# Kernel optimization log

Hardware: AMD Instinct MI355X
Metric: run time of the kernel (lower is better)

## Reference

```python
import jax, jax.numpy as jnp
import numpy as np

B, FR, D = 32, 300, 2048
E, G, K = 2, 8, 64
FEAT = E * D // G          # 512
VLAD = K * FEAT            # 32768
H, R = 2048, 8
NC = 3862
BN_EPS = 1e-5
L2_EPS = 1e-12


def _bn(x, g, b, m, v):
    # eval-mode BatchNorm1d with running stats
    return (x - m) * jax.lax.rsqrt(v + BN_EPS) * g + b


def _l2n(x, axis):
    # torch F.normalize: x / max(||x||, eps)
    n = jnp.sqrt(jnp.sum(x * x, axis=axis, keepdims=True))
    return x / jnp.maximum(n, L2_EPS)


def setup_inputs() -> dict:
    key = jax.random.key(0)
    ks = jax.random.split(key, 10)
    rn = lambda k, s: jax.random.normal(k, s, jnp.float32) * 0.02
    return {
        "x": jax.random.normal(ks[0], (B, FR, D), jnp.float32),
        "fc1_w": rn(ks[1], (E * D, D)), "fc1_b": jnp.zeros((E * D,), jnp.float32),
        "fc2_w": rn(ks[2], (G, E * D)), "fc2_b": jnp.zeros((G,), jnp.float32),
        "c1": jax.random.uniform(ks[3], (E * D, G * K), jnp.float32),
        "c2": jax.random.uniform(ks[4], (1, FEAT, K), jnp.float32),
        "bn1_g": jnp.ones((G * K,), jnp.float32), "bn1_b": jnp.zeros((G * K,), jnp.float32),
        "bn1_m": jnp.zeros((G * K,), jnp.float32), "bn1_v": jnp.ones((G * K,), jnp.float32),
        "bn2_g": jnp.ones((VLAD,), jnp.float32), "bn2_b": jnp.zeros((VLAD,), jnp.float32),
        "bn2_m": jnp.zeros((VLAD,), jnp.float32), "bn2_v": jnp.ones((VLAD,), jnp.float32),
        "cgf_w": rn(ks[5], (H, VLAD)), "cgf_b": jnp.zeros((H,), jnp.float32),
        "cgbn_g": jnp.ones((H,), jnp.float32), "cgbn_b": jnp.zeros((H,), jnp.float32),
        "cgbn_m": jnp.zeros((H,), jnp.float32), "cgbn_v": jnp.ones((H,), jnp.float32),
        "g1_w": rn(ks[6], (H // R, H)), "g1_b": jnp.zeros((H // R,), jnp.float32),
        "gbn_g": jnp.ones((H // R,), jnp.float32), "gbn_b": jnp.zeros((H // R,), jnp.float32),
        "gbn_m": jnp.zeros((H // R,), jnp.float32), "gbn_v": jnp.ones((H // R,), jnp.float32),
        "g2_w": rn(ks[7], (H, H // R)), "g2_b": jnp.zeros((H,), jnp.float32),
        "fc3_w": rn(ks[8], (NC, H)), "fc3_b": jnp.zeros((NC,), jnp.float32),
    }


def _forward(x, fc1_w, fc1_b, fc2_w, fc2_b, c1, c2,
             bn1_g, bn1_b, bn1_m, bn1_v, bn2_g, bn2_b, bn2_m, bn2_v,
             cgf_w, cgf_b, cgbn_g, cgbn_b, cgbn_m, cgbn_v,
             g1_w, g1_b, gbn_g, gbn_b, gbn_m, gbn_v, g2_w, g2_b, fc3_w, fc3_b):
    b, fr, d = x.shape
    xn = _l2n(x, 2)                                      # per-frame L2 normalize
    h = xn @ fc1_w.T + fc1_b                             # [B,FR,E*D]
    att = jax.nn.sigmoid(h @ fc2_w.T + fc2_b)            # [B,FR,G]
    att = att.reshape(b, fr * G, 1)
    act = jnp.einsum('bfd,dc->bfc', h, c1)               # [B,FR,G*K]
    act = _bn(act, bn1_g, bn1_b, bn1_m, bn1_v)
    act = act.reshape(b, fr * G, K)
    act = jax.nn.softmax(act, axis=-1) * att             # soft-assign * attention
    a = act.sum(axis=1, keepdims=True) * c2              # [B,FEAT,K] via broadcast
    res = h.reshape(b, fr * G, FEAT)
    vlad = jnp.einsum('bnk,bnf->bfk', act, res) - a      # [B,FEAT,K]
    vlad = _l2n(vlad, 1).reshape(b, VLAD)                # intra-norm, flatten feat-major
    vlad = _bn(vlad, bn2_g, bn2_b, bn2_m, bn2_v)
    # SE context gating (dropout identity in reference)
    y = _bn(vlad @ cgf_w.T + cgf_b, cgbn_g, cgbn_b, cgbn_m, cgbn_v)   # [B,H]
    gate = jax.nn.sigmoid(
        jax.nn.relu(_bn(y @ g1_w.T + g1_b, gbn_g, gbn_b, gbn_m, gbn_v)) @ g2_w.T + g2_b)
    return (y * gate) @ fc3_w.T + fc3_b                  # [B,NC]


def reference(x, fc1_w, fc1_b, fc2_w, fc2_b, c1, c2,
              bn1_g, bn1_b, bn1_m, bn1_v, bn2_g, bn2_b, bn2_m, bn2_v,
              cgf_w, cgf_b, cgbn_g, cgbn_b, cgbn_m, cgbn_v,
              g1_w, g1_b, gbn_g, gbn_b, gbn_m, gbn_v, g2_w, g2_b, fc3_w, fc3_b):
    return _forward(x, fc1_w, fc1_b, fc2_w, fc2_b, c1, c2,
                    bn1_g, bn1_b, bn1_m, bn1_v, bn2_g, bn2_b, bn2_m, bn2_v,
                    cgf_w, cgf_b, cgbn_g, cgbn_b, cgbn_m, cgbn_v,
                    g1_w, g1_b, gbn_g, gbn_b, gbn_m, gbn_v, g2_w, g2_b, fc3_w, fc3_b)
```

## Files before the change

### kernel.cpp

```cpp
#include <hip/hip_runtime.h>

typedef unsigned short u16;
typedef unsigned int u32;
using f32x4 = __attribute__((ext_vector_type(4))) float;
using s16x8 = __attribute__((ext_vector_type(8))) short;
using u16x4 = __attribute__((ext_vector_type(4))) u16;

#define DEV __device__ __forceinline__

DEV float bf2f(u16 u) { union { u32 i; float f; } v; v.i = ((u32)u) << 16; return v.f; }
DEV u16 f2bf(float f) {
  union { float ff; u32 uu; } v; v.ff = f;
  u32 r = (v.uu + 0x7fffu + ((v.uu >> 16) & 1u)) >> 16;
  return (u16)r;
}

DEV void gl_lds16(const void* g, void* l) {
  __builtin_amdgcn_global_load_lds(
      (const __attribute__((address_space(1))) u32*)g,
      (__attribute__((address_space(3))) u32*)l, 16, 0, 0);
}

__global__ __launch_bounds__(256) void k_l2norm(const float* __restrict__ x, u16* __restrict__ xn) {
  int r = blockIdx.x, t = threadIdx.x;
  const float* xr = x + (size_t)r * 2048;
  float v[8], s = 0.f;
#pragma unroll
  for (int i = 0; i < 8; i++) { v[i] = xr[t + i*256]; s += v[i]*v[i]; }
#pragma unroll
  for (int off = 32; off > 0; off >>= 1) s += __shfl_xor(s, off, 64);
  __shared__ float red[4];
  if ((t & 63) == 0) red[t >> 6] = s;
  __syncthreads();
  float inv = 1.f / fmaxf(sqrtf(red[0]+red[1]+red[2]+red[3]), 1e-12f);
  u16* xo = xn + (size_t)r * 2048;
#pragma unroll
  for (int i = 0; i < 8; i++) xo[t + i*256] = f2bf(v[i]*inv);
}

__global__ void k_cvt(const float* __restrict__ in, u16* __restrict__ out, int n4) {
  int i = blockIdx.x*256 + threadIdx.x, st = gridDim.x*256;
  for (; i < n4; i += st) {
    f32x4 v = ((const f32x4*)in)[i];
    u16x4 o;
    o[0] = f2bf(v[0]); o[1] = f2bf(v[1]); o[2] = f2bf(v[2]); o[3] = f2bf(v[3]);
    ((u16x4*)out)[i] = o;
  }
}

__global__ __launch_bounds__(256) void k_transpose(const float* __restrict__ c1, u16* __restrict__ c1t) {
  __shared__ float tile[32][33];
  int k0 = blockIdx.x*32, n0 = blockIdx.y*32;
  int tx = threadIdx.x & 31, ty = threadIdx.x >> 5;
  for (int i = ty; i < 32; i += 8) tile[i][tx] = c1[(size_t)(k0+i)*512 + n0 + tx];
  __syncthreads();
  for (int i = ty; i < 32; i += 8) c1t[(size_t)(n0+i)*4096 + k0 + tx] = f2bf(tile[tx][i]);
}

template<bool WF32, bool WBF16>
__global__ __launch_bounds__(256) void k_gemm(
    const u16* __restrict__ A, const u16* __restrict__ Bt, const float* __restrict__ bias,
    float* __restrict__ Cf, u16* __restrict__ Cb, int N, int K, int Nlim,
    int MT, int NT, int swz) {
  __shared__ u16 As[128*32];
  __shared__ u16 Bs[128*32];
  int bid = blockIdx.x, mt, nt;
  if (swz) {
    int mg = (MT + 7) >> 3;
    int gid = bid >> 5, gl = bid & 31;
    mt = (gid % mg)*8 + (gl & 7);
    nt = (gid / mg)*4 + (gl >> 3);
    if (mt >= MT) return;
  } else { mt = bid % MT; nt = bid / MT; }
  int t = threadIdx.x, wv = t >> 6;
  int quad = (t & 63) >> 4, lr = t & 15;
  size_t m0 = (size_t)mt * 128, n0 = (size_t)nt * 128;
  int wm = wv & 1, wn = wv >> 1;
  int srow = t >> 2;
  int scol = (((t & 3) ^ ((t >> 3) & 3)) * 8);
  const u16* gA = A + (m0 + srow)*(size_t)K + scol;
  const u16* gB = Bt + (n0 + srow)*(size_t)K + scol;
  u16* lA = &As[wv*512];
  u16* lB = &Bs[wv*512];
  int xq = (quad ^ ((lr >> 1) & 3)) * 8;
  f32x4 acc[4][4];
#pragma unroll
  for (int i = 0; i < 4; i++)
#pragma unroll
    for (int j = 0; j < 4; j++) acc[i][j] = (f32x4){0.f,0.f,0.f,0.f};
  for (int k0 = 0; k0 < K; k0 += 32) {
    gl_lds16(gA + k0, lA);
    gl_lds16(gA + (size_t)64*K + k0, lA + 2048);
    gl_lds16(gB + k0, lB);
    gl_lds16(gB + (size_t)64*K + k0, lB + 2048);
    __syncthreads();
    s16x8 af[4], bfr[4];
#pragma unroll
    for (int i = 0; i < 4; i++) {
      af[i]  = *(const s16x8*)&As[(wm*64 + i*16 + lr)*32 + xq];
      bfr[i] = *(const s16x8*)&Bs[(wn*64 + i*16 + lr)*32 + xq];
    }
#pragma unroll
    for (int i = 0; i < 4; i++)
#pragma unroll
      for (int j = 0; j < 4; j++)
        acc[i][j] = __builtin_amdgcn_mfma_f32_16x16x32_bf16(af[i], bfr[j], acc[i][j], 0, 0, 0);
    __syncthreads();
  }
#pragma unroll
  for (int j = 0; j < 4; j++) {
    size_t nn = n0 + wn*64 + j*16 + lr;
    if ((int)nn >= Nlim) continue;
    float bj = bias ? bias[nn] : 0.f;
#pragma unroll
    for (int i = 0; i < 4; i++) {
      size_t mr = m0 + wm*64 + i*16 + quad*4;
#pragma unroll
      for (int r = 0; r < 4; r++) {
        float v = acc[i][j][r] + bj;
        if (WF32)  Cf[(mr + r)*N + nn] = v;
        if (WBF16) Cb[(mr + r)*N + nn] = f2bf(v);
      }
    }
  }
}

__global__ __launch_bounds__(256) void k_hbt(const u16* __restrict__ hb, u16* __restrict__ hbT) {
  __shared__ u16 tile[64*33];
  int nt = blockIdx.x, ft = blockIdx.y, b = blockIdx.z, t = threadIdx.x;
  int n0 = nt*32, f0 = ft*64;
  int rrel = t >> 6, g = (t >> 3) & 7, fi = (t & 7)*8;
  const u16* src = hb + ((size_t)(b*300 + (n0 >> 3) + rrel))*4096 + g*512 + f0 + fi;
  u16 v[8];
  *(u16x4*)v = *(const u16x4*)src;
  *(u16x4*)(v+4) = *(const u16x4*)(src+4);
  int nl = rrel*8 + g;
#pragma unroll
  for (int e = 0; e < 8; e++) tile[(fi+e)*33 + nl] = v[e];
  __syncthreads();
  int f = t >> 2, nc = (t & 3)*8;
  u16 o[8];
#pragma unroll
  for (int e = 0; e < 8; e++) o[e] = tile[f*33 + nc + e];
  u16* dst = hbT + ((size_t)b*512 + f0 + f)*2400 + n0 + nc;
  *(u16x4*)dst = *(u16x4*)o;
  *(u16x4*)(dst+4) = *(u16x4*)(o+4);
}

__global__ __launch_bounds__(512) void k_softmax(const float* __restrict__ act_ext,
    const float* __restrict__ fc2_b,
    const float* __restrict__ g, const float* __restrict__ b,
    const float* __restrict__ mu, const float* __restrict__ var, u16* __restrict__ actT) {
  int m = blockIdx.x, t = threadIdx.x;
  int bb = m / 300, fr = m - bb*300;
  int gi = t >> 6, k = t & 63, c = t;
  float v = act_ext[(size_t)m*640 + c];
  v = (v - mu[c]) * rsqrtf(var[c] + 1e-5f) * g[c] + b[c];
  float mx = v;
#pragma unroll
  for (int off = 32; off > 0; off >>= 1) mx = fmaxf(mx, __shfl_xor(mx, off, 64));
  float e = __expf(v - mx);
  float s = e;
#pragma unroll
  for (int off = 32; off > 0; off >>= 1) s += __shfl_xor(s, off, 64);
  float attl = act_ext[(size_t)m*640 + 512 + gi] + fc2_b[gi];
  float attv = 1.f / (1.f + __expf(-attl));
  float r = (e / s) * attv;
  __shared__ u16 st[64*9];
  st[k*9 + gi] = f2bf(r);
  __syncthreads();
  if (t < 64) {
    u16 o[8];
#pragma unroll
    for (int e2 = 0; e2 < 8; e2++) o[e2] = st[t*9 + e2];
    u16* dst = actT + ((size_t)bb*64 + t)*2400 + fr*8;
    *(u16x4*)dst = *(u16x4*)o;
    *(u16x4*)(dst+4) = *(u16x4*)(o+4);
  }
}

__global__ __launch_bounds__(256) void k_asum(const u16* __restrict__ actT, float* __restrict__ a_sum) {
  int b = blockIdx.x, t = threadIdx.x;
  int k = t >> 2, q = t & 3;
  const u16* p = actT + ((size_t)b*64 + k)*2400 + q*600;
  float acc = 0.f;
  for (int j = 0; j < 600; j += 8) {
    u16x4 a0 = *(const u16x4*)(p + j);
    u16x4 a1 = *(const u16x4*)(p + j + 4);
    acc += bf2f(a0[0])+bf2f(a0[1])+bf2f(a0[2])+bf2f(a0[3])
         + bf2f(a1[0])+bf2f(a1[1])+bf2f(a1[2])+bf2f(a1[3]);
  }
  __shared__ float red[256];
  red[t] = acc;
  __syncthreads();
  if (t < 64) a_sum[b*64 + t] = red[t*4] + red[t*4+1] + red[t*4+2] + red[t*4+3];
}

__global__ __launch_bounds__(256) void k_vlad(const u16* __restrict__ hbT, const u16* __restrict__ actT,
                                              float* __restrict__ P2) {
  __shared__ u16 As[128*32];
  __shared__ u16 Bs[64*32];
  int t = threadIdx.x, wv = t >> 6;
  int quad = (t & 63) >> 4, lr = t & 15;
  int ft = blockIdx.x, b = blockIdx.y, ns = blockIdx.z;
  int wm = wv & 1, wn = wv >> 1;
  int srow = t >> 2;
  int scol = (((t & 3) ^ ((t >> 3) & 3)) * 8);
  int xq = (quad ^ ((lr >> 1) & 3)) * 8;
  const u16* gA = hbT + ((size_t)b*512 + ft*128 + srow)*2400 + ns*480 + scol;
  const u16* gB = actT + ((size_t)b*64 + srow)*2400 + ns*480 + scol;
  u16* lA = &As[wv*512];
  u16* lB = &Bs[wv*512];
  f32x4 acc[4][2];
#pragma unroll
  for (int i = 0; i < 4; i++)
#pragma unroll
    for (int j = 0; j < 2; j++) acc[i][j] = (f32x4){0.f,0.f,0.f,0.f};
  for (int k0 = 0; k0 < 480; k0 += 32) {
    gl_lds16(gA + k0, lA);
    gl_lds16(gA + (size_t)64*2400 + k0, lA + 2048);
    gl_lds16(gB + k0, lB);
    __syncthreads();
    s16x8 af[4], bfr[2];
#pragma unroll
    for (int i = 0; i < 4; i++)
      af[i] = *(const s16x8*)&As[(wm*64 + i*16 + lr)*32 + xq];
#pragma unroll
    for (int j = 0; j < 2; j++)
      bfr[j] = *(const s16x8*)&Bs[(wn*32 + j*16 + lr)*32 + xq];
#pragma unroll
    for (int i = 0; i < 4; i++)
#pragma unroll
      for (int j = 0; j < 2; j++)
        acc[i][j] = __builtin_amdgcn_mfma_f32_16x16x32_bf16(af[i], bfr[j], acc[i][j], 0, 0, 0);
    __syncthreads();
  }
  size_t base = ((size_t)ns*32 + b)*512*64;
#pragma unroll
  for (int j = 0; j < 2; j++) {
    int kc = wn*32 + j*16 + lr;
#pragma unroll
    for (int i = 0; i < 4; i++) {
      int f = ft*128 + wm*64 + i*16 + quad*4;
#pragma unroll
      for (int r = 0; r < 4; r++)
        P2[base + (size_t)(f + r)*64 + kc] = acc[i][j][r];
    }
  }
}

__global__ __launch_bounds__(256) void k_norm2(const float* __restrict__ P2, const float* __restrict__ a_sum,
    const float* __restrict__ c2, const float* __restrict__ g, const float* __restrict__ b,
    const float* __restrict__ mu, const float* __restrict__ var, float* __restrict__ out) {
  int k = blockIdx.x, bb = blockIdx.y, t = threadIdx.x;
  float as = a_sum[bb*64 + k];
  int f0 = t, f1 = t + 256;
  const size_t PS = (size_t)32*512*64;
  size_t base = (size_t)bb*512*64;
  float x0 = 0.f, x1 = 0.f;
#pragma unroll
  for (int ns = 0; ns < 5; ns++) {
    x0 += P2[ns*PS + base + (size_t)f0*64 + k];
    x1 += P2[ns*PS + base + (size_t)f1*64 + k];
  }
  x0 -= as * c2[f0*64 + k];
  x1 -= as * c2[f1*64 + k];
  float s = x0*x0 + x1*x1;
#pragma unroll
  for (int off = 32; off > 0; off >>= 1) s += __shfl_xor(s, off, 64);
  __shared__ float red[4];
  if ((t & 63) == 0) red[t >> 6] = s;
  __syncthreads();
  float inv = 1.f / fmaxf(sqrtf(red[0]+red[1]+red[2]+red[3]), 1e-12f);
  int c0 = f0*64 + k, c1 = f1*64 + k;
  out[(size_t)bb*32768 + c0] = (x0*inv - mu[c0]) * rsqrtf(var[c0]+1e-5f) * g[c0] + b[c0];
  out[(size_t)bb*32768 + c1] = (x1*inv - mu[c1]) * rsqrtf(var[c1]+1e-5f) * g[c1] + b[c1];
}

__global__ __launch_bounds__(256) void k_skgemm(
    const float* __restrict__ A, const float* __restrict__ W,
    float* __restrict__ P, int N, int K, int KC, int Npad) {
  constexpr int LDB = 72;
  __shared__ u16 Bs[128*LDB];
  __shared__ u16 As[32*LDB];
  int t = threadIdx.x;
  int wv = t >> 6, quad = (t & 63) >> 4, lr = t & 15;
  int n0 = blockIdx.x * 128;
  size_t kc0 = (size_t)blockIdx.y * KC;
  f32x4 acc[2][2];
#pragma unroll
  for (int i = 0; i < 2; i++)
#pragma unroll
    for (int j = 0; j < 2; j++) acc[i][j] = (f32x4){0.f,0.f,0.f,0.f};
  int wl[8]; size_t wg[8];
#pragma unroll
  for (int i = 0; i < 8; i++) {
    int slot = i*256 + t;
    int r = slot >> 4, q = slot & 15;
    int row = n0 + r; if (row >= N) row = N - 1;
    wl[i] = r*LDB + q*4;
    wg[i] = (size_t)row*K + kc0 + q*4;
  }
  int al[2]; size_t ag[2];
#pragma unroll
  for (int i = 0; i < 2; i++) {
    int slot = i*256 + t;
    int r = slot >> 4, q = slot & 15;
    al[i] = r*LDB + q*4;
    ag[i] = (size_t)r*K + kc0 + q*4;
  }
  int nst = KC >> 6;
  f32x4 wv4[8], av4[2];
#pragma unroll
  for (int i = 0; i < 8; i++) wv4[i] = *(const f32x4*)(W + wg[i]);
#pragma unroll
  for (int i = 0; i < 2; i++) av4[i] = *(const f32x4*)(A + ag[i]);
  for (int s = 0; s < nst; s++) {
    if (s) __syncthreads();
#pragma unroll
    for (int i = 0; i < 8; i++) {
      u16x4 o;
      o[0] = f2bf(wv4[i][0]); o[1] = f2bf(wv4[i][1]);
      o[2] = f2bf(wv4[i][2]); o[3] = f2bf(wv4[i][3]);
      *(u16x4*)&Bs[wl[i]] = o;
    }
#pragma unroll
    for (int i = 0; i < 2; i++) {
      u16x4 o;
      o[0] = f2bf(av4[i][0]); o[1] = f2bf(av4[i][1]);
      o[2] = f2bf(av4[i][2]); o[3] = f2bf(av4[i][3]);
      *(u16x4*)&As[al[i]] = o;
    }
    __syncthreads();
    if (s + 1 < nst) {
      int off = (s + 1) * 64;
#pragma unroll
      for (int i = 0; i < 8; i++) wv4[i] = *(const f32x4*)(W + wg[i] + off);
#pragma unroll
      for (int i = 0; i < 2; i++) av4[i] = *(const f32x4*)(A + ag[i] + off);
    }
#pragma unroll
    for (int ks = 0; ks < 2; ks++) {
      s16x8 af[2];
#pragma unroll
      for (int i = 0; i < 2; i++)
        af[i] = *(const s16x8*)&As[(i*16 + lr)*LDB + ks*32 + quad*8];
#pragma unroll
      for (int j = 0; j < 2; j++) {
        s16x8 bf = *(const s16x8*)&Bs[(wv*32 + j*16 + lr)*LDB + ks*32 + quad*8];
#pragma unroll
        for (int i = 0; i < 2; i++)
          acc[i][j] = __builtin_amdgcn_mfma_f32_16x16x32_bf16(af[i], bf, acc[i][j], 0, 0, 0);
      }
    }
  }
#pragma unroll
  for (int i = 0; i < 2; i++)
#pragma unroll
    for (int j = 0; j < 2; j++) {
      int n = n0 + wv*32 + j*16 + lr;
#pragma unroll
      for (int r = 0; r < 4; r++) {
        int m = i*16 + quad*4 + r;
        P[((size_t)blockIdx.y*32 + m)*Npad + n] = acc[i][j][r];
      }
    }
}

template<int EPI>
__global__ __launch_bounds__(256) void k_skred(const float* __restrict__ P, int KSPLIT, int N, int Npad,
    const float* __restrict__ bias, const float* __restrict__ bg, const float* __restrict__ bb,
    const float* __restrict__ bm, const float* __restrict__ bv, float* __restrict__ C) {
  int idx = blockIdx.x*256 + threadIdx.x;
  if (idx >= 32*N) return;
  int m = idx / N, n = idx - m*N;
  float s = 0.f;
  for (int k = 0; k < KSPLIT; k++) s += P[((size_t)k*32 + m)*Npad + n];
  float v = s + (bias ? bias[n] : 0.f);
  if (EPI == 1 || EPI == 2) {
    v = (v - bm[n]) * rsqrtf(bv[n] + 1e-5f) * bg[n] + bb[n];
    if (EPI == 2) v = fmaxf(v, 0.f);
  } else if (EPI == 3) {
    v = 1.f / (1.f + __expf(-v));
  }
  C[idx] = v;
}

__global__ void k_mul(const float* __restrict__ a, const float* __restrict__ b, float* __restrict__ o, int n) {
  int i = blockIdx.x*256 + threadIdx.x;
  if (i < n) o[i] = a[i]*b[i];
}

extern "C" void kernel_launch(void* const* d_in, const int* in_sizes, int n_in,
                              void* d_out, int out_size, void* d_ws, size_t ws_size,
                              hipStream_t stream) {
  (void)in_sizes; (void)n_in; (void)out_size; (void)ws_size;
  const float* x      = (const float*)d_in[0];
  const float* fc1_w  = (const float*)d_in[1];
  const float* fc1_b  = (const float*)d_in[2];
  const float* fc2_w  = (const float*)d_in[3];
  const float* fc2_b  = (const float*)d_in[4];
  const float* c1     = (const float*)d_in[5];
  const float* c2     = (const float*)d_in[6];
  const float* bn1_g  = (const float*)d_in[7];
  const float* bn1_b  = (const float*)d_in[8];
  const float* bn1_m  = (const float*)d_in[9];
  const float* bn1_v  = (const float*)d_in[10];
  const float* bn2_g  = (const float*)d_in[11];
  const float* bn2_b  = (const float*)d_in[12];
  const float* bn2_m  = (const float*)d_in[13];
  const float* bn2_v  = (const float*)d_in[14];
  const float* cgf_w  = (const float*)d_in[15];
  const float* cgf_b  = (const float*)d_in[16];
  const float* cgbn_g = (const float*)d_in[17];
  const float* cgbn_b = (const float*)d_in[18];
  const float* cgbn_m = (const float*)d_in[19];
  const float* cgbn_v = (const float*)d_in[20];
  const float* g1_w   = (const float*)d_in[21];
  const float* g1_b   = (const float*)d_in[22];
  const float* gbn_g  = (const float*)d_in[23];
  const float* gbn_b  = (const float*)d_in[24];
  const float* gbn_m  = (const float*)d_in[25];
  const float* gbn_v  = (const float*)d_in[26];
  const float* g2_w   = (const float*)d_in[27];
  const float* g2_b   = (const float*)d_in[28];
  const float* fc3_w  = (const float*)d_in[29];
  const float* fc3_b  = (const float*)d_in[30];

  char* w = (char*)d_ws;
  u16*   xn    = (u16*)  (w + 0);
  u16*   w1b   = (u16*)  (w + 39321600);
  u16*   hbT   = (u16*)  (w + 0);
  u16*   hb    = (u16*)  (w + 78643200);
  u16*   c1ext = (u16*)  (w + 157286400);
  float* actx  = (float*)(w + 162529280);
  u16*   actT  = (u16*)  (w + 187105280);
  float* P2    = (float*)(w + 196935680);
  float* P     = (float*)(w + 196935680);
  float* a_sum = (float*)(w + 217907200);
  float* vladn = (float*)(w + 217915392);
  float* y     = (float*)(w + 222109696);
  float* z     = (float*)(w + 222371840);
  float* gate  = (float*)(w + 222404608);
  float* yg    = (float*)(w + 222666752);

  k_l2norm<<<9600, 256, 0, stream>>>(x, xn);
  k_cvt<<<2048, 256, 0, stream>>>(fc1_w, w1b, (4096*2048)/4);
  k_transpose<<<dim3(128, 16), 256, 0, stream>>>(c1, c1ext);
  k_cvt<<<32, 256, 0, stream>>>(fc2_w, c1ext + (size_t)512*4096, (8*4096)/4);
  k_gemm<false, true><<<2560, 256, 0, stream>>>(xn, w1b, fc1_b, nullptr, hb, 4096, 2048, 4096, 75, 32, 1);
  k_hbt<<<dim3(75, 8, 32), 256, 0, stream>>>(hb, hbT);
  k_gemm<true, false><<<375, 256, 0, stream>>>(hb, c1ext, nullptr, actx, nullptr, 640, 4096, 520, 75, 5, 0);
  k_softmax<<<9600, 512, 0, stream>>>(actx, fc2_b, bn1_g, bn1_b, bn1_m, bn1_v, actT);
  k_asum<<<32, 256, 0, stream>>>(actT, a_sum);
  k_vlad<<<dim3(4, 32, 5), 256, 0, stream>>>(hbT, actT, P2);
  k_norm2<<<dim3(64, 32), 256, 0, stream>>>(P2, a_sum, c2, bn2_g, bn2_b, bn2_m, bn2_v, vladn);

  k_skgemm<<<dim3(16, 64), 256, 0, stream>>>(vladn, cgf_w, P, 2048, 32768, 512, 2048);
  k_skred<1><<<256, 256, 0, stream>>>(P, 64, 2048, 2048, cgf_b, cgbn_g, cgbn_b, cgbn_m, cgbn_v, y);
  k_skgemm<<<dim3(2, 32), 256, 0, stream>>>(y, g1_w, P, 256, 2048, 64, 256);
  k_skred<2><<<32, 256, 0, stream>>>(P, 32, 256, 256, g1_b, gbn_g, gbn_b, gbn_m, gbn_v, z);
  k_skgemm<<<dim3(16, 4), 256, 0, stream>>>(z, g2_w, P, 2048, 256, 64, 2048);
  k_skred<3><<<256, 256, 0, stream>>>(P, 4, 2048, 2048, g2_b, nullptr, nullptr, nullptr, nullptr, gate);
  k_mul<<<256, 256, 0, stream>>>(y, gate, yg, 65536);
  k_skgemm<<<dim3(31, 16), 256, 0, stream>>>(yg, fc3_w, P, 3862, 2048, 128, 3968);
  k_skred<0><<<483, 256, 0, stream>>>(P, 16, 3862, 3968, fc3_b, nullptr, nullptr, nullptr, nullptr, (float*)d_out);
}
```

Baseline: 1.012 ms.

## Add 256x256-tile 8-wave MFMA GEMM with ping-pong LDS for fc1

Adds a new bf16 MFMA GEMM kernel that uses 256x256 output tiles, 512 threads and double-buffered LDS filled by direct global-to-LDS loads. Loads are staggered across the K loop with explicit vmcnt waits, barriers and s_setprio around MFMA bursts. It replaces the 128-tile GEMM for the fc1 projection (9600x4096x2048). The aim is more data reuse per tile and better overlap of loads with MFMA work. In exchange it needs 128KB of LDS per block, which limits occupancy, and the last M tile reads A rows past the 9600 valid rows (stores are guarded).

```diff
diff --git a/kernel.cpp b/kernel.cpp
--- a/kernel.cpp
+++ b/kernel.cpp
@@ -20,6 +20,13 @@
       (const __attribute__((address_space(1))) u32*)g,
       (__attribute__((address_space(3))) u32*)l, 16, 0, 0);
 }
+
+DEV void BAR() { __builtin_amdgcn_s_barrier(); }
+DEV void LGKM0() { asm volatile("s_waitcnt lgkmcnt(0)" ::: "memory"); __builtin_amdgcn_sched_barrier(0); }
+DEV void VM6() { asm volatile("s_waitcnt vmcnt(6)" ::: "memory"); }
+DEV void VM0() { asm volatile("s_waitcnt vmcnt(0)" ::: "memory"); }
+DEV void PRIO1() { __builtin_amdgcn_s_setprio(1); }
+DEV void PRIO0() { __builtin_amdgcn_s_setprio(0); }
 
 __global__ __launch_bounds__(256) void k_l2norm(const float* __restrict__ x, u16* __restrict__ xn) {
   int r = blockIdx.x, t = threadIdx.x;
@@ -120,6 +127,131 @@
         float v = acc[i][j][r] + bj;
         if (WF32)  Cf[(mr + r)*N + nn] = v;
         if (WBF16) Cb[(mr + r)*N + nn] = f2bf(v);
+      }
+    }
+  }
+}
+
+template<bool WF32, bool WBF16>
+__global__ __launch_bounds__(512, 2) void k_gemm256(
+    const u16* __restrict__ A, const u16* __restrict__ Bt, const float* __restrict__ bias,
+    float* __restrict__ Cf, u16* __restrict__ Cb,
+    int M, int N, int K, int Nlim, int MT, int NT, int swz) {
+  constexpr int TILE = 256*64;
+  __shared__ u16 lds[4*TILE];
+  int bid = blockIdx.x;
+  if (swz) { int c = (MT*NT) >> 3; bid = (bid & 7)*c + (bid >> 3); }
+  int mt = bid % MT, nt = bid / MT;
+  int t = threadIdx.x, wv = t >> 6, lane = t & 63;
+  int quad = lane >> 4, lr = lane & 15;
+  int wm = wv >> 2, wn = wv & 3;
+  size_t m0 = (size_t)mt * 256, n0 = (size_t)nt * 256;
+  int srow = wv*8 + (lane >> 3);
+  int schunk = ((lane & 7) ^ (lane >> 3)) * 8;
+  const u16* gA = A  + (size_t)(m0 + srow)*K + schunk;
+  const u16* gB = Bt + (size_t)(n0 + srow)*K + schunk;
+  size_t row64 = (size_t)64 * K;
+  int lofs = wv*512;
+  int raBase = (wm*128 + lr)*64;
+  int rbBase = (wn*64  + lr)*64;
+  int pc0 = ((0 + quad) ^ (lr & 7)) * 8;
+  int pc1 = ((4 + quad) ^ (lr & 7)) * 8;
+  f32x4 acc[8][4];
+#pragma unroll
+  for (int i = 0; i < 8; i++)
+#pragma unroll
+    for (int j = 0; j < 4; j++) acc[i][j] = (f32x4){0.f,0.f,0.f,0.f};
+
+  int T = K >> 6;
+  u16* A0 = lds;            u16* B0 = lds + TILE;
+  u16* A1 = lds + 2*TILE;   u16* B1 = lds + 3*TILE;
+#pragma unroll
+  for (int q = 0; q < 4; q++) gl_lds16(gA + q*row64, A0 + q*4096 + lofs);
+#pragma unroll
+  for (int q = 0; q < 4; q++) gl_lds16(gB + q*row64, B0 + q*4096 + lofs);
+#pragma unroll
+  for (int q = 0; q < 4; q++) gl_lds16(gA + 64 + q*row64, A1 + q*4096 + lofs);
+  gl_lds16(gB + 64 + 0*row64, B1 + 0*4096 + lofs);
+  gl_lds16(gB + 64 + 1*row64, B1 + 1*4096 + lofs);
+  VM6();
+  BAR();
+
+  for (int tt = 0; tt < T; ++tt) {
+    u16* Ac = lds + (tt & 1)*(2*TILE);
+    u16* Bc = Ac + TILE;
+    u16* Bn = lds + ((tt + 1) & 1)*(2*TILE) + TILE;
+    s16x8 a[8], b[4];
+#pragma unroll
+    for (int i = 0; i < 8; i++) a[i] = *(const s16x8*)&Ac[raBase + i*1024 + pc0];
+#pragma unroll
+    for (int j = 0; j < 4; j++) b[j] = *(const s16x8*)&Bc[rbBase + j*1024 + pc0];
+    if (tt + 1 < T) {
+      const u16* gB1 = gB + (size_t)(tt + 1)*64;
+      gl_lds16(gB1 + 2*row64, Bn + 2*4096 + lofs);
+      gl_lds16(gB1 + 3*row64, Bn + 3*4096 + lofs);
+    }
+    BAR(); LGKM0();
+    PRIO1();
+#pragma unroll
+    for (int i = 0; i < 8; i++) {
+      acc[i][0] = __builtin_amdgcn_mfma_f32_16x16x32_bf16(a[i], b[0], acc[i][0], 0, 0, 0);
+      acc[i][1] = __builtin_amdgcn_mfma_f32_16x16x32_bf16(a[i], b[1], acc[i][1], 0, 0, 0);
+    }
+    PRIO0(); BAR();
+    PRIO1();
+#pragma unroll
+    for (int i = 0; i < 8; i++) {
+      acc[i][2] = __builtin_amdgcn_mfma_f32_16x16x32_bf16(a[i], b[2], acc[i][2], 0, 0, 0);
+      acc[i][3] = __builtin_amdgcn_mfma_f32_16x16x32_bf16(a[i], b[3], acc[i][3], 0, 0, 0);
+    }
+    PRIO0(); BAR();
+#pragma unroll
+    for (int i = 0; i < 8; i++) a[i] = *(const s16x8*)&Ac[raBase + i*1024 + pc1];
+#pragma unroll
+    for (int j = 0; j < 4; j++) b[j] = *(const s16x8*)&Bc[rbBase + j*1024 + pc1];
+    BAR(); LGKM0();
+    PRIO1();
+#pragma unroll
+    for (int i = 0; i < 8; i++) {
+      acc[i][0] = __builtin_amdgcn_mfma_f32_16x16x32_bf16(a[i], b[0], acc[i][0], 0, 0, 0);
+      acc[i][1] = __builtin_amdgcn_mfma_f32_16x16x32_bf16(a[i], b[1], acc[i][1], 0, 0, 0);
+    }
+    PRIO0(); BAR();
+    if (tt + 2 < T) {
+      const u16* gA2 = gA + (size_t)(tt + 2)*64;
+      const u16* gB2 = gB + (size_t)(tt + 2)*64;
+#pragma unroll
+      for (int q = 0; q < 4; q++) gl_lds16(gA2 + q*row64, Ac + q*4096 + lofs);
+      gl_lds16(gB2 + 0*row64, Bc + 0*4096 + lofs);
+      gl_lds16(gB2 + 1*row64, Bc + 1*4096 + lofs);
+    }
+    BAR();
+    PRIO1();
+#pragma unroll
+    for (int i = 0; i < 8; i++) {
+      acc[i][2] = __builtin_amdgcn_mfma_f32_16x16x32_bf16(a[i], b[2], acc[i][2], 0, 0, 0);
+      acc[i][3] = __builtin_amdgcn_mfma_f32_16x16x32_bf16(a[i], b[3], acc[i][3], 0, 0, 0);
+    }
+    PRIO0();
+    if (tt + 2 < T) VM6();
+    else if (tt + 1 < T) VM0();
+    BAR();
+  }
+
+#pragma unroll
+  for (int j = 0; j < 4; j++) {
+    int nn = (int)n0 + wn*64 + j*16 + lr;
+    if (nn >= Nlim) continue;
+    float bj = bias ? bias[nn] : 0.f;
+#pragma unroll
+    for (int i = 0; i < 8; i++) {
+      int mr = (int)m0 + wm*128 + i*16 + quad*4;
+#pragma unroll
+      for (int r = 0; r < 4; r++) {
+        if (mr + r >= M) continue;
+        float v = acc[i][j][r] + bj;
+        if (WF32)  Cf[(size_t)(mr + r)*N + nn] = v;
+        if (WBF16) Cb[(size_t)(mr + r)*N + nn] = f2bf(v);
       }
     }
   }
@@ -448,7 +580,8 @@
   k_cvt<<<2048, 256, 0, stream>>>(fc1_w, w1b, (4096*2048)/4);
   k_transpose<<<dim3(128, 16), 256, 0, stream>>>(c1, c1ext);
   k_cvt<<<32, 256, 0, stream>>>(fc2_w, c1ext + (size_t)512*4096, (8*4096)/4);
-  k_gemm<false, true><<<2560, 256, 0, stream>>>(xn, w1b, fc1_b, nullptr, hb, 4096, 2048, 4096, 75, 32, 1);
+  k_gemm256<false, true><<<608, 512, 0, stream>>>(xn, w1b, fc1_b, nullptr, hb,
+                                                  9600, 4096, 2048, 4096, 38, 16, 1);
   k_hbt<<<dim3(75, 8, 32), 256, 0, stream>>>(hb, hbT);
   k_gemm<true, false><<<375, 256, 0, stream>>>(hb, c1ext, nullptr, actx, nullptr, 640, 4096, 520, 75, 5, 0);
   k_softmax<<<9600, 512, 0, stream>>>(actx, fc2_b, bn1_g, bn1_b, bn1_m, bn1_v, actT);
```

Result: no change. 1.021 ms (+0.8%).
